# Kernel tuning notes

Hardware: AMD Instinct MI355X
Metric: run time of the kernel (lower is better)

The kernel has to match this reference:

```python
import jax, jax.numpy as jnp
import numpy as np

RADIUS = 0.4
K = 32
EPS = 1e-5


def ball_query(xyz, new_xyz, radius, k):
    """xyz: (B,N,3), new_xyz: (B,M,3) -> idx (B,M,k) int32.
    Replicates CUDA ball_query: first k points within radius (in index order),
    padded with the first found index."""
    N = xyz.shape[1]
    # squared distances (B,M,N)
    d2 = jnp.sum((new_xyz[:, :, None, :] - xyz[:, None, :, :]) ** 2, axis=-1)
    within = d2 < radius * radius
    order = jnp.arange(N, dtype=jnp.int32)
    key = jnp.where(within, order[None, None, :], N)
    idx_sorted = jnp.argsort(key, axis=-1)[..., :k].astype(jnp.int32)  # (B,M,k)
    cnt = within.sum(axis=-1)  # (B,M)
    first = idx_sorted[..., :1]
    slot = jnp.arange(k)[None, None, :]
    return jnp.where(slot < cnt[..., None], idx_sorted, first)


def gather_bmk(x_bnc, idx):
    """x_bnc: (B,N,C), idx: (B,M,K) -> (B,M,K,C)"""
    return jnp.take_along_axis(x_bnc[:, None, :, :], idx[..., None], axis=2)


def conv_bn_relu(x, w, b, gamma, beta):
    """x: (B,Cin,M,K); w: (Cout,Cin). 1x1 Conv2d + BatchNorm2d (train stats) + ReLU."""
    x = jnp.einsum('bcmk,oc->bomk', x, w) + b[None, :, None, None]
    mu = x.mean(axis=(0, 2, 3), keepdims=True)
    var = x.var(axis=(0, 2, 3), keepdims=True)
    x = gamma[None, :, None, None] * (x - mu) * jax.lax.rsqrt(var + EPS) + beta[None, :, None, None]
    return jax.nn.relu(x)


def setup_inputs() -> dict:
    key = jax.random.key(0)
    ks = jax.random.split(key, 16)
    B, N, C, M = 4, 16384, 128, 1024
    mlp = [131, 128, 128, 256]
    inp = {
        'points_xyz': jax.random.normal(ks[0], (B, N, 3), dtype=jnp.float32),
        'features': jax.random.normal(ks[1], (B, C, N), dtype=jnp.float32),
        'indices': jax.random.randint(ks[2], (B, M), 0, N, dtype=jnp.int32),
    }
    for i in range(3):
        cin, cout = mlp[i], mlp[i + 1]
        inp[f'w{i+1}'] = jax.random.normal(ks[3 + 4 * i], (cout, cin), dtype=jnp.float32) / np.sqrt(cin)
        inp[f'b{i+1}'] = jnp.zeros((cout,), dtype=jnp.float32)
        inp[f'g{i+1}'] = jnp.ones((cout,), dtype=jnp.float32)
        inp[f'beta{i+1}'] = jnp.zeros((cout,), dtype=jnp.float32)
    return inp


def reference(points_xyz, features, indices,
              w1, b1, g1, beta1, w2, b2, g2, beta2, w3, b3, g3, beta3):
    # sample centers: new_xyz (B,M,3)
    new_xyz = jnp.take_along_axis(points_xyz, indices[..., None], axis=1)
    # ball query + group
    idx = ball_query(points_xyz, new_xyz, RADIUS, K)            # (B,M,K)
    grouped_xyz = gather_bmk(points_xyz, idx) - new_xyz[:, :, None, :]  # (B,M,K,3)
    grouped_feat = gather_bmk(features.transpose(0, 2, 1), idx)         # (B,M,K,C)
    x = jnp.concatenate([grouped_xyz, grouped_feat], axis=-1)           # (B,M,K,3+C)
    x = x.transpose(0, 3, 1, 2)                                         # (B,3+C,M,K)
    # shared MLP (1x1 Conv2d + BN + ReLU)
    x = conv_bn_relu(x, w1, b1, g1, beta1)
    x = conv_bn_relu(x, w2, b2, g2, beta2)
    x = conv_bn_relu(x, w3, b3, g3, beta3)
    # max pool over K -> (B, Cout, M)
    new_features = x.max(axis=-1)
    return new_xyz, new_features
```

## Files before the change

### kernel.cpp

```cpp
#include <hip/hip_runtime.h>

#define B_ 4
#define N_ 16384
#define C_ 128
#define M_ 1024
#define K_ 32
#define NTOT (B_*M_*K_)
#define RAD2 0.16f
#define EPS_ 1e-5f

typedef unsigned short ushort_t;
typedef __bf16 bf16x8 __attribute__((ext_vector_type(8)));
typedef float f32x4 __attribute__((ext_vector_type(4)));

__device__ __forceinline__ float b2f(ushort_t u){
  unsigned int x = ((unsigned int)u) << 16;
  return __builtin_bit_cast(float, x);
}
__device__ __forceinline__ ushort_t f2b(float f){
  unsigned int u = __builtin_bit_cast(unsigned int, f);
  unsigned int r = (u + 0x7FFFu + ((u >> 16) & 1u)) >> 16;
  return (ushort_t)r;
}

__global__ __launch_bounds__(256) void ball_query_k(
    const float* __restrict__ xyz, const int* __restrict__ indices,
    float* __restrict__ new_xyz, int* __restrict__ idx)
{
  int t = threadIdx.x;
  int wv = t >> 6, lane = t & 63;
  int g = blockIdx.x*4 + wv;
  int b = g >> 10;
  const float* pb = xyz + (size_t)b*N_*3;
  const float4* pb4 = (const float4*)pb;
  int qi = indices[g];
  float qx = pb[qi*3+0], qy = pb[qi*3+1], qz = pb[qi*3+2];
  if (lane < 3) new_xyz[g*3 + lane] = pb[qi*3 + lane];

  int cnt = 0, firstIdx = 0;
  int* op = idx + g*K_;

  float4 buf0[6], buf1[6];
  #pragma unroll
  for (int i = 0; i < 6; i++) buf0[i] = pb4[lane*6 + i];

  auto process = [&](const float4* buf, int chunk){
    const float* f = (const float*)buf;
    unsigned int local_mask = 0;
    #pragma unroll
    for (int j = 0; j < 8; j++){
      float dx = f[j*3+0]-qx, dy = f[j*3+1]-qy, dz = f[j*3+2]-qz;
      if (dx*dx + dy*dy + dz*dz < RAD2) local_mask |= (1u << j);
    }
    if (__ballot(local_mask != 0) == 0ull) return;
    int base = chunk*512;
    int lcnt = __popc(local_mask);
    int incl = lcnt;
    #pragma unroll
    for (int d = 1; d < 64; d <<= 1){
      int tt = __shfl_up(incl, d);
      if (lane >= d) incl += tt;
    }
    int excl = incl - lcnt;
    int total = __shfl(incl, 63);
    if (cnt == 0){
      int lf = local_mask ? (lane*8 + __builtin_ctz(local_mask)) : 0x7fffffff;
      #pragma unroll
      for (int d = 1; d < 64; d <<= 1) lf = min(lf, __shfl_xor(lf, d));
      firstIdx = base + lf;
    }
    int sl = cnt + excl;
    unsigned int m = local_mask;
    while (m && sl < K_){
      int j = __builtin_ctz(m); m &= m - 1u;
      op[sl++] = base + lane*8 + j;
    }
    cnt += total;
  };

  for (int chunk = 0; chunk < 32; chunk += 2){
    if (chunk + 1 < 32){
      #pragma unroll
      for (int i = 0; i < 6; i++) buf1[i] = pb4[(chunk+1)*384 + lane*6 + i];
    }
    process(buf0, chunk);
    if (cnt >= K_) break;
    if (chunk + 2 < 32){
      #pragma unroll
      for (int i = 0; i < 6; i++) buf0[i] = pb4[(chunk+2)*384 + lane*6 + i];
    }
    process(buf1, chunk + 1);
    if (cnt >= K_) break;
  }
  if (cnt < K_){
    for (int s = cnt + lane; s < K_; s += 64) op[s] = firstIdx;
  }
}

__global__ __launch_bounds__(256) void transpose_feat_k(
    const float* __restrict__ feat, ushort_t* __restrict__ ftr_t)
{
  __shared__ float T[32][133];
  int bi = blockIdx.x;
  int b = bi >> 9, ntile = bi & 511;
  int n0 = ntile * 32;
  int t = threadIdx.x;
  int nl = t & 31;
  #pragma unroll
  for (int ci = 0; ci < 16; ci++){
    int c = ci*8 + (t >> 5);
    T[nl][c] = feat[((size_t)b*C_ + c)*N_ + n0 + nl];
  }
  __syncthreads();
  #pragma unroll
  for (int ii = 0; ii < 2; ii++){
    int v = ii*256 + t;
    int n2 = v >> 4, seg = v & 15;
    union { ushort_t u[8]; uint4 q; } pk;
    #pragma unroll
    for (int j = 0; j < 8; j++) pk.u[j] = f2b(T[n2][seg*8 + j]);
    *(uint4*)(ftr_t + ((size_t)b*N_ + n0 + n2)*C_ + seg*8) = pk.q;
  }
}

__global__ __launch_bounds__(256) void prep_w_k(
    const float* __restrict__ w1, const float* __restrict__ w2, const float* __restrict__ w3,
    ushort_t* __restrict__ W1b, ushort_t* __restrict__ W2b, ushort_t* __restrict__ W3b)
{
  const int T1 = 128*160, T2 = 128*128, T3 = 256*128;
  for (int e = blockIdx.x*256 + threadIdx.x; e < T1+T2+T3; e += gridDim.x*256){
    if (e < T1){
      int o = e / 160, c = e % 160;
      float v = 0.f;
      if (c < 128) v = w1[o*131 + 3 + c];
      else if (c < 131) v = w1[o*131 + (c - 128)];
      W1b[e] = f2b(v);
    } else if (e < T1+T2){
      int e2 = e - T1;
      W2b[e2] = f2b(w2[e2]);
    } else {
      int e3 = e - T1 - T2;
      W3b[e3] = f2b(w3[e3]);
    }
  }
}

__global__ __launch_bounds__(256, 2) void conv1_k(
    const float* __restrict__ xyz, const ushort_t* __restrict__ ftr_t,
    const int* __restrict__ idx, const float* __restrict__ new_xyz,
    const ushort_t* __restrict__ W1b, const float* __restrict__ b1,
    ushort_t* __restrict__ Y1, float* __restrict__ sumO, float* __restrict__ sqO)
{
  __shared__ alignas(16) ushort_t Xs[32*168];
  __shared__ alignas(16) float Ys[32*132];
  int t = threadIdx.x;
  int wv = t >> 6, lane = t & 63, quad = lane >> 4, l15 = lane & 15;
  int row = t >> 3, chunk = t & 7;

  if (t < 128){
    int rr = t >> 2, cc = t & 3;
    *(uint4*)(Xs + rr*168 + 128 + cc*8) = make_uint4(0,0,0,0);
  }
  bf16x8 wf[2][5];
  #pragma unroll
  for (int nt = 0; nt < 2; nt++)
    #pragma unroll
    for (int kt = 0; kt < 5; kt++)
      wf[nt][kt] = *(const bf16x8*)(W1b + (wv*32 + nt*16 + l15)*160 + kt*32 + quad*8);
  float bs_r[2] = { b1[wv*32 + l15], b1[wv*32 + 16 + l15] };
  float s[2] = {0.f,0.f}, s2[2] = {0.f,0.f};

  const int GPB = 8;
  int g0 = blockIdx.x * GPB;
  int b = g0 >> 10;
  int ia[GPB], ibv[GPB];
  #pragma unroll
  for (int i = 0; i < GPB; i++){
    ia[i]  = idx[(g0+i)*K_ + row];
    ibv[i] = idx[(g0+i)*K_ + (t & 31)];
  }
  for (int i = 0; i < GPB; i++){
    int g = g0 + i;
    const ushort_t* src = ftr_t + ((size_t)b*N_ + ia[i])*C_ + chunk*16;
    uint4 q0 = *(const uint4*)src;
    uint4 q1 = *(const uint4*)(src + 8);
    *(uint4*)(Xs + row*168 + chunk*16) = q0;
    *(uint4*)(Xs + row*168 + chunk*16 + 8) = q1;
    if (t < 32){
      const float* pp = xyz + ((size_t)b*N_ + ibv[i])*3;
      const float* qq = new_xyz + (size_t)g*3;
      unsigned int u0 = (unsigned int)f2b(pp[0]-qq[0]) | ((unsigned int)f2b(pp[1]-qq[1]) << 16);
      unsigned int u1 = (unsigned int)f2b(pp[2]-qq[2]);
      *(uint2*)(Xs + t*168 + 128) = make_uint2(u0, u1);
    }
    __syncthreads();
    bf16x8 af[2][5];
    #pragma unroll
    for (int mt = 0; mt < 2; mt++)
      #pragma unroll
      for (int kt = 0; kt < 5; kt++)
        af[mt][kt] = *(const bf16x8*)(Xs + (mt*16 + l15)*168 + kt*32 + quad*8);
    f32x4 acc[2][2];
    #pragma unroll
    for (int nt = 0; nt < 2; nt++){ acc[nt][0] = (f32x4){0,0,0,0}; acc[nt][1] = (f32x4){0,0,0,0}; }
    #pragma unroll
    for (int nt = 0; nt < 2; nt++)
      #pragma unroll
      for (int kt = 0; kt < 5; kt++){
        acc[nt][0] = __builtin_amdgcn_mfma_f32_16x16x32_bf16(af[0][kt], wf[nt][kt], acc[nt][0], 0,0,0);
        acc[nt][1] = __builtin_amdgcn_mfma_f32_16x16x32_bf16(af[1][kt], wf[nt][kt], acc[nt][1], 0,0,0);
      }
    #pragma unroll
    for (int nt = 0; nt < 2; nt++){
      int o = wv*32 + nt*16 + l15;
      #pragma unroll
      for (int mt = 0; mt < 2; mt++)
        #pragma unroll
        for (int r = 0; r < 4; r++){
          float v = acc[nt][mt][r] + bs_r[nt];
          s[nt] += v; s2[nt] += v*v;
          Ys[(mt*16 + quad*4 + r)*132 + o] = v;
        }
    }
    __syncthreads();
    {
      const float* yp = &Ys[row*132 + chunk*16];
      f32x4 y0 = *(const f32x4*)(yp);
      f32x4 y1 = *(const f32x4*)(yp + 4);
      f32x4 y2 = *(const f32x4*)(yp + 8);
      f32x4 y3 = *(const f32x4*)(yp + 12);
      union { ushort_t u[8]; uint4 q; } p0, p1;
      #pragma unroll
      for (int j = 0; j < 4; j++){
        p0.u[j] = f2b(y0[j]); p0.u[4+j] = f2b(y1[j]);
        p1.u[j] = f2b(y2[j]); p1.u[4+j] = f2b(y3[j]);
      }
      ushort_t* dst = Y1 + ((size_t)g*K_ + row)*128 + chunk*16;
      *(uint4*)dst = p0.q;
      *(uint4*)(dst + 8) = p1.q;
    }
  }
  #pragma unroll
  for (int nt = 0; nt < 2; nt++){
    s[nt]  += __shfl_xor(s[nt], 16);  s[nt]  += __shfl_xor(s[nt], 32);
    s2[nt] += __shfl_xor(s2[nt], 16); s2[nt] += __shfl_xor(s2[nt], 32);
    if (quad == 0){
      int o = wv*32 + nt*16 + l15;
      atomicAdd(&sumO[o], s[nt]);
      atomicAdd(&sqO[o], s2[nt]);
    }
  }
}

template<int COUT, bool MAXMIN>
__global__ __launch_bounds__(256, 2) void convB_k(
    const ushort_t* __restrict__ Yin, const ushort_t* __restrict__ Wb,
    const float* __restrict__ bias, const float* __restrict__ g_bn,
    const float* __restrict__ beta_bn, const float* __restrict__ sumI,
    const float* __restrict__ sqI, ushort_t* __restrict__ Yout,
    unsigned int* __restrict__ Ymm, float* __restrict__ sumO, float* __restrict__ sqO)
{
  constexpr int NT = COUT/64;
  constexpr int NXS = MAXMIN ? 2 : 1;
  __shared__ alignas(16) ushort_t Xs[NXS][32*136];
  __shared__ alignas(16) float Ys[MAXMIN ? 4 : 32*132];
  int t = threadIdx.x;
  int wv = t >> 6, lane = t & 63, quad = lane >> 4, l15 = lane & 15;
  int row = t >> 3, chunk = t & 7;

  float a_r[16], d_r[16];
  #pragma unroll
  for (int j = 0; j < 16; j++){
    int c = chunk*16 + j;
    float mu  = sumI[c] * (1.f/NTOT);
    float var = sqI[c]  * (1.f/NTOT) - mu*mu;
    float a = g_bn[c] * rsqrtf(var + EPS_);
    a_r[j] = a; d_r[j] = beta_bn[c] - a*mu;
  }
  bf16x8 wf[NT][4];
  #pragma unroll
  for (int nt = 0; nt < NT; nt++)
    #pragma unroll
    for (int kt = 0; kt < 4; kt++)
      wf[nt][kt] = *(const bf16x8*)(Wb + (wv*(NT*16) + nt*16 + l15)*128 + kt*32 + quad*8);
  float bs_r[NT];
  #pragma unroll
  for (int nt = 0; nt < NT; nt++) bs_r[nt] = bias[wv*(NT*16) + nt*16 + l15];
  float s[NT], s2[NT];
  #pragma unroll
  for (int nt = 0; nt < NT; nt++){ s[nt] = 0.f; s2[nt] = 0.f; }

  const int GPB = 8;
  int g0 = blockIdx.x * GPB;
  uint4 r0, r1;
  {
    const ushort_t* src = Yin + ((size_t)g0*K_ + row)*128 + chunk*16;
    r0 = *(const uint4*)src; r1 = *(const uint4*)(src + 8);
  }
  for (int i = 0; i < GPB; i++){
    int g = g0 + i;
    ushort_t* X = Xs[MAXMIN ? (i & (NXS-1)) : 0];
    union { ushort_t u[8]; uint4 q; } i0, i1, o0, o1;
    i0.q = r0; i1.q = r1;
    #pragma unroll
    for (int j = 0; j < 8; j++){
      o0.u[j] = f2b(fmaxf(a_r[j]  *b2f(i0.u[j]) + d_r[j],   0.f));
      o1.u[j] = f2b(fmaxf(a_r[8+j]*b2f(i1.u[j]) + d_r[8+j], 0.f));
    }
    *(uint4*)(X + row*136 + chunk*16) = o0.q;
    *(uint4*)(X + row*136 + chunk*16 + 8) = o1.q;
    if (i + 1 < GPB){
      const ushort_t* src = Yin + ((size_t)(g+1)*K_ + row)*128 + chunk*16;
      r0 = *(const uint4*)src; r1 = *(const uint4*)(src + 8);
    }
    __syncthreads();
    bf16x8 af[2][4];
    #pragma unroll
    for (int mt = 0; mt < 2; mt++)
      #pragma unroll
      for (int kt = 0; kt < 4; kt++)
        af[mt][kt] = *(const bf16x8*)(X + (mt*16 + l15)*136 + kt*32 + quad*8);
    f32x4 acc[NT][2];
    #pragma unroll
    for (int nt = 0; nt < NT; nt++){ acc[nt][0] = (f32x4){0,0,0,0}; acc[nt][1] = (f32x4){0,0,0,0}; }
    #pragma unroll
    for (int nt = 0; nt < NT; nt++)
      #pragma unroll
      for (int kt = 0; kt < 4; kt++){
        acc[nt][0] = __builtin_amdgcn_mfma_f32_16x16x32_bf16(af[0][kt], wf[nt][kt], acc[nt][0], 0,0,0);
        acc[nt][1] = __builtin_amdgcn_mfma_f32_16x16x32_bf16(af[1][kt], wf[nt][kt], acc[nt][1], 0,0,0);
      }
    if constexpr (!MAXMIN){
      #pragma unroll
      for (int nt = 0; nt < NT; nt++){
        int o = wv*(NT*16) + nt*16 + l15;
        #pragma unroll
        for (int mt = 0; mt < 2; mt++)
          #pragma unroll
          for (int r = 0; r < 4; r++){
            float v = acc[nt][mt][r] + bs_r[nt];
            s[nt] += v; s2[nt] += v*v;
            Ys[(mt*16 + quad*4 + r)*132 + o] = v;
          }
      }
      __syncthreads();
      const float* yp = &Ys[row*132 + chunk*16];
      f32x4 y0 = *(const f32x4*)(yp);
      f32x4 y1 = *(const f32x4*)(yp + 4);
      f32x4 y2 = *(const f32x4*)(yp + 8);
      f32x4 y3 = *(const f32x4*)(yp + 12);
      union { ushort_t u[8]; uint4 q; } p0, p1;
      #pragma unroll
      for (int j = 0; j < 4; j++){
        p0.u[j] = f2b(y0[j]); p0.u[4+j] = f2b(y1[j]);
        p1.u[j] = f2b(y2[j]); p1.u[4+j] = f2b(y3[j]);
      }
      ushort_t* dst = Yout + ((size_t)g*K_ + row)*128 + chunk*16;
      *(uint4*)dst = p0.q;
      *(uint4*)(dst + 8) = p1.q;
    } else {
      #pragma unroll
      for (int nt = 0; nt < NT; nt++){
        float v0 = acc[nt][0][0] + bs_r[nt];
        float mx = v0, mn = v0;
        s[nt] += v0; s2[nt] += v0*v0;
        #pragma unroll
        for (int mt = 0; mt < 2; mt++)
          #pragma unroll
          for (int r = 0; r < 4; r++){
            if (mt == 0 && r == 0) continue;
            float v = acc[nt][mt][r] + bs_r[nt];
            s[nt] += v; s2[nt] += v*v;
            mx = fmaxf(mx, v); mn = fminf(mn, v);
          }
        mx = fmaxf(mx, __shfl_xor(mx, 16)); mx = fmaxf(mx, __shfl_xor(mx, 32));
        mn = fminf(mn, __shfl_xor(mn, 16)); mn = fminf(mn, __shfl_xor(mn, 32));
        if (quad == 0){
          int o = wv*64 + nt*16 + l15;
          Ymm[(size_t)g*256 + o] = (unsigned int)f2b(mx) | ((unsigned int)f2b(mn) << 16);
        }
      }
    }
  }
  #pragma unroll
  for (int nt = 0; nt < NT; nt++){
    s[nt]  += __shfl_xor(s[nt], 16);  s[nt]  += __shfl_xor(s[nt], 32);
    s2[nt] += __shfl_xor(s2[nt], 16); s2[nt] += __shfl_xor(s2[nt], 32);
    if (quad == 0){
      int o = wv*(NT*16) + nt*16 + l15;
      atomicAdd(&sumO[o], s[nt]);
      atomicAdd(&sqO[o], s2[nt]);
    }
  }
}

__global__ __launch_bounds__(256) void finalize_k(
    const unsigned int* __restrict__ Ymm, const float* __restrict__ g3,
    const float* __restrict__ beta3, const float* __restrict__ sum3,
    const float* __restrict__ sq3, float* __restrict__ out)
{
  __shared__ float T[16][264];
  __shared__ float abn[256], dbn[256];
  int t = threadIdx.x;
  int b = blockIdx.x >> 6;
  int m0 = (blockIdx.x & 63) * 16;
  {
    float mu  = sum3[t] * (1.f/NTOT);
    float var = sq3[t]  * (1.f/NTOT) - mu*mu;
    float a = g3[t] * rsqrtf(var + EPS_);
    abn[t] = a; dbn[t] = beta3[t] - a*mu;
  }
  __syncthreads();
  #pragma unroll
  for (int i = 0; i < 4; i++){
    int v4 = i*256 + t;
    int m = v4 >> 6, oq = (v4 & 63) * 4;
    uint4 w = *(const uint4*)(Ymm + ((size_t)(b*M_ + m0 + m))*256 + oq);
    unsigned int wsv[4] = {w.x, w.y, w.z, w.w};
    float r[4];
    #pragma unroll
    for (int j = 0; j < 4; j++){
      int o = oq + j;
      float mx = b2f((ushort_t)(wsv[j] & 0xffffu));
      float mn = b2f((ushort_t)(wsv[j] >> 16));
      float a = abn[o];
      float val = (a >= 0.f) ? (a*mx + dbn[o]) : (a*mn + dbn[o]);
      r[j] = fmaxf(val, 0.f);
    }
    *(f32x4*)(&T[m][oq]) = *(f32x4*)r;
  }
  __syncthreads();
  #pragma unroll
  for (int p = 0; p < 4; p++){
    int o = p*64 + (t >> 2), c = t & 3;
    float4 v = make_float4(T[c*4+0][o], T[c*4+1][o], T[c*4+2][o], T[c*4+3][o]);
    *(float4*)(out + ((size_t)(b*256 + o))*M_ + m0 + c*4) = v;
  }
}

extern "C" void kernel_launch(void* const* d_in, const int* in_sizes, int n_in,
                              void* d_out, int out_size, void* d_ws, size_t ws_size,
                              hipStream_t stream)
{
  (void)in_sizes; (void)n_in; (void)out_size; (void)ws_size;
  const float* xyz  = (const float*)d_in[0];
  const float* feat = (const float*)d_in[1];
  const int*   inds = (const int*)d_in[2];
  const float* w1 = (const float*)d_in[3];
  const float* b1 = (const float*)d_in[4];
  const float* g1 = (const float*)d_in[5];
  const float* be1= (const float*)d_in[6];
  const float* w2 = (const float*)d_in[7];
  const float* b2 = (const float*)d_in[8];
  const float* g2 = (const float*)d_in[9];
  const float* be2= (const float*)d_in[10];
  const float* w3 = (const float*)d_in[11];
  const float* b3 = (const float*)d_in[12];
  const float* g3 = (const float*)d_in[13];
  const float* be3= (const float*)d_in[14];

  char* ws = (char*)d_ws;
  float* stats = (float*)ws;
  float* s1sum = stats + 0*256;  float* s1sq = stats + 1*256;
  float* s2sum = stats + 2*256;  float* s2sq = stats + 3*256;
  float* s3sum = stats + 4*256;  float* s3sq = stats + 5*256;
  size_t off = 6*256*sizeof(float);
  int* idx = (int*)(ws + off);                off += (size_t)B_*M_*K_*4;
  ushort_t* ftr_t = (ushort_t*)(ws + off);    off += (size_t)B_*N_*C_*2;
  ushort_t* W1b = (ushort_t*)(ws + off);      off += 128*160*2;
  ushort_t* W2b = (ushort_t*)(ws + off);      off += 128*128*2;
  ushort_t* W3b = (ushort_t*)(ws + off);      off += 256*128*2;
  ushort_t* Y1 = (ushort_t*)(ws + off);       off += (size_t)NTOT*128*2;
  ushort_t* Y2 = (ushort_t*)(ws + off);       off += (size_t)NTOT*128*2;
  unsigned int* Ymm = (unsigned int*)(ws + off); off += (size_t)B_*M_*256*4;

  float* new_xyz  = (float*)d_out;
  float* out_feat = (float*)d_out + (size_t)B_*M_*3;

  hipMemsetAsync(stats, 0, 6*256*sizeof(float), stream);
  prep_w_k<<<272, 256, 0, stream>>>(w1, w2, w3, W1b, W2b, W3b);
  transpose_feat_k<<<2048, 256, 0, stream>>>(feat, ftr_t);
  ball_query_k<<<1024, 256, 0, stream>>>(xyz, inds, new_xyz, idx);
  conv1_k<<<512, 256, 0, stream>>>(xyz, ftr_t, idx, new_xyz, W1b, b1, Y1, s1sum, s1sq);
  convB_k<128,false><<<512, 256, 0, stream>>>(Y1, W2b, b2, g1, be1, s1sum, s1sq, Y2, nullptr, s2sum, s2sq);
  convB_k<256,true ><<<512, 256, 0, stream>>>(Y2, W3b, b3, g2, be2, s2sum, s2sq, nullptr, Ymm, s3sum, s3sq);
  finalize_k<<<256, 256, 0, stream>>>(Ymm, g3, be3, s3sum, s3sq, out_feat);
}
```

Baseline: 225.0 us.

## Split conv output channels across two blocks to double grid size

Each conv kernel now covers half of the output channels per block, and the grid doubles from 512 to 1024 blocks. The goal is more parallelism and occupancy on a GPU with many CUs, plus less register and LDS pressure per block. The cost is that every block still gathers and normalizes the full 32x(128/160) input tile, so the gather and input-side work is done twice. Atomic stat updates per block also double.

```diff
diff --git a/kernel.cpp b/kernel.cpp
--- a/kernel.cpp
+++ b/kernel.cpp
@@ -152,26 +152,26 @@
     ushort_t* __restrict__ Y1, float* __restrict__ sumO, float* __restrict__ sqO)
 {
   __shared__ alignas(16) ushort_t Xs[32*168];
-  __shared__ alignas(16) float Ys[32*132];
+  __shared__ alignas(16) float Ys[32*68];
   int t = threadIdx.x;
   int wv = t >> 6, lane = t & 63, quad = lane >> 4, l15 = lane & 15;
   int row = t >> 3, chunk = t & 7;
+  int col0 = (blockIdx.x & 1) * 64;
+  int blk = blockIdx.x >> 1;
 
   if (t < 128){
     int rr = t >> 2, cc = t & 3;
     *(uint4*)(Xs + rr*168 + 128 + cc*8) = make_uint4(0,0,0,0);
   }
-  bf16x8 wf[2][5];
-  #pragma unroll
-  for (int nt = 0; nt < 2; nt++)
-    #pragma unroll
-    for (int kt = 0; kt < 5; kt++)
-      wf[nt][kt] = *(const bf16x8*)(W1b + (wv*32 + nt*16 + l15)*160 + kt*32 + quad*8);
-  float bs_r[2] = { b1[wv*32 + l15], b1[wv*32 + 16 + l15] };
-  float s[2] = {0.f,0.f}, s2[2] = {0.f,0.f};
+  bf16x8 wf[5];
+  #pragma unroll
+  for (int kt = 0; kt < 5; kt++)
+    wf[kt] = *(const bf16x8*)(W1b + (col0 + wv*16 + l15)*160 + kt*32 + quad*8);
+  float bs_r = b1[col0 + wv*16 + l15];
+  float s = 0.f, s2 = 0.f;
 
   const int GPB = 8;
-  int g0 = blockIdx.x * GPB;
+  int g0 = blk * GPB;
   int b = g0 >> 10;
   int ia[GPB], ibv[GPB];
   #pragma unroll
@@ -200,55 +200,42 @@
       #pragma unroll
       for (int kt = 0; kt < 5; kt++)
         af[mt][kt] = *(const bf16x8*)(Xs + (mt*16 + l15)*168 + kt*32 + quad*8);
-    f32x4 acc[2][2];
-    #pragma unroll
-    for (int nt = 0; nt < 2; nt++){ acc[nt][0] = (f32x4){0,0,0,0}; acc[nt][1] = (f32x4){0,0,0,0}; }
-    #pragma unroll
-    for (int nt = 0; nt < 2; nt++)
-      #pragma unroll
-      for (int kt = 0; kt < 5; kt++){
-        acc[nt][0] = __builtin_amdgcn_mfma_f32_16x16x32_bf16(af[0][kt], wf[nt][kt], acc[nt][0], 0,0,0);
-        acc[nt][1] = __builtin_amdgcn_mfma_f32_16x16x32_bf16(af[1][kt], wf[nt][kt], acc[nt][1], 0,0,0);
-      }
-    #pragma unroll
-    for (int nt = 0; nt < 2; nt++){
-      int o = wv*32 + nt*16 + l15;
+    f32x4 acc[2] = {(f32x4){0,0,0,0}, (f32x4){0,0,0,0}};
+    #pragma unroll
+    for (int kt = 0; kt < 5; kt++){
+      acc[0] = __builtin_amdgcn_mfma_f32_16x16x32_bf16(af[0][kt], wf[kt], acc[0], 0,0,0);
+      acc[1] = __builtin_amdgcn_mfma_f32_16x16x32_bf16(af[1][kt], wf[kt], acc[1], 0,0,0);
+    }
+    {
+      int o = wv*16 + l15;
       #pragma unroll
       for (int mt = 0; mt < 2; mt++)
         #pragma unroll
         for (int r = 0; r < 4; r++){
-          float v = acc[nt][mt][r] + bs_r[nt];
-          s[nt] += v; s2[nt] += v*v;
-          Ys[(mt*16 + quad*4 + r)*132 + o] = v;
+          float v = acc[mt][r] + bs_r;
+          s += v; s2 += v*v;
+          Ys[(mt*16 + quad*4 + r)*68 + o] = v;
         }
     }
     __syncthreads();
     {
-      const float* yp = &Ys[row*132 + chunk*16];
+      const float* yp = &Ys[row*68 + chunk*8];
       f32x4 y0 = *(const f32x4*)(yp);
       f32x4 y1 = *(const f32x4*)(yp + 4);
-      f32x4 y2 = *(const f32x4*)(yp + 8);
-      f32x4 y3 = *(const f32x4*)(yp + 12);
-      union { ushort_t u[8]; uint4 q; } p0, p1;
+      union { ushort_t u[8]; uint4 q; } p0;
       #pragma unroll
       for (int j = 0; j < 4; j++){
         p0.u[j] = f2b(y0[j]); p0.u[4+j] = f2b(y1[j]);
-        p1.u[j] = f2b(y2[j]); p1.u[4+j] = f2b(y3[j]);
       }
-      ushort_t* dst = Y1 + ((size_t)g*K_ + row)*128 + chunk*16;
-      *(uint4*)dst = p0.q;
-      *(uint4*)(dst + 8) = p1.q;
-    }
-  }
-  #pragma unroll
-  for (int nt = 0; nt < 2; nt++){
-    s[nt]  += __shfl_xor(s[nt], 16);  s[nt]  += __shfl_xor(s[nt], 32);
-    s2[nt] += __shfl_xor(s2[nt], 16); s2[nt] += __shfl_xor(s2[nt], 32);
-    if (quad == 0){
-      int o = wv*32 + nt*16 + l15;
-      atomicAdd(&sumO[o], s[nt]);
-      atomicAdd(&sqO[o], s2[nt]);
-    }
+      *(uint4*)(Y1 + ((size_t)g*K_ + row)*128 + col0 + chunk*8) = p0.q;
+    }
+  }
+  s  += __shfl_xor(s, 16);  s  += __shfl_xor(s, 32);
+  s2 += __shfl_xor(s2, 16); s2 += __shfl_xor(s2, 32);
+  if (quad == 0){
+    int o = col0 + wv*16 + l15;
+    atomicAdd(&sumO[o], s);
+    atomicAdd(&sqO[o], s2);
   }
 }
 
@@ -260,13 +247,16 @@
     const float* __restrict__ sqI, ushort_t* __restrict__ Yout,
     unsigned int* __restrict__ Ymm, float* __restrict__ sumO, float* __restrict__ sqO)
 {
-  constexpr int NT = COUT/64;
+  constexpr int HALF = COUT/2;
+  constexpr int NT = HALF/64;
   constexpr int NXS = MAXMIN ? 2 : 1;
   __shared__ alignas(16) ushort_t Xs[NXS][32*136];
-  __shared__ alignas(16) float Ys[MAXMIN ? 4 : 32*132];
+  __shared__ alignas(16) float Ys[MAXMIN ? 4 : 32*68];
   int t = threadIdx.x;
   int wv = t >> 6, lane = t & 63, quad = lane >> 4, l15 = lane & 15;
   int row = t >> 3, chunk = t & 7;
+  int col0 = (blockIdx.x & 1) * HALF;
+  int blk = blockIdx.x >> 1;
 
   float a_r[16], d_r[16];
   #pragma unroll
@@ -282,16 +272,16 @@
   for (int nt = 0; nt < NT; nt++)
     #pragma unroll
     for (int kt = 0; kt < 4; kt++)
-      wf[nt][kt] = *(const bf16x8*)(Wb + (wv*(NT*16) + nt*16 + l15)*128 + kt*32 + quad*8);
+      wf[nt][kt] = *(const bf16x8*)(Wb + (col0 + wv*(NT*16) + nt*16 + l15)*128 + kt*32 + quad*8);
   float bs_r[NT];
   #pragma unroll
-  for (int nt = 0; nt < NT; nt++) bs_r[nt] = bias[wv*(NT*16) + nt*16 + l15];
+  for (int nt = 0; nt < NT; nt++) bs_r[nt] = bias[col0 + wv*(NT*16) + nt*16 + l15];
   float s[NT], s2[NT];
   #pragma unroll
   for (int nt = 0; nt < NT; nt++){ s[nt] = 0.f; s2[nt] = 0.f; }
 
   const int GPB = 8;
-  int g0 = blockIdx.x * GPB;
+  int g0 = blk * GPB;
   uint4 r0, r1;
   {
     const ushort_t* src = Yin + ((size_t)g0*K_ + row)*128 + chunk*16;
@@ -331,33 +321,27 @@
         acc[nt][1] = __builtin_amdgcn_mfma_f32_16x16x32_bf16(af[1][kt], wf[nt][kt], acc[nt][1], 0,0,0);
       }
     if constexpr (!MAXMIN){
-      #pragma unroll
-      for (int nt = 0; nt < NT; nt++){
-        int o = wv*(NT*16) + nt*16 + l15;
+      {
+        int o = wv*16 + l15;
         #pragma unroll
         for (int mt = 0; mt < 2; mt++)
           #pragma unroll
           for (int r = 0; r < 4; r++){
-            float v = acc[nt][mt][r] + bs_r[nt];
-            s[nt] += v; s2[nt] += v*v;
-            Ys[(mt*16 + quad*4 + r)*132 + o] = v;
+            float v = acc[0][mt][r] + bs_r[0];
+            s[0] += v; s2[0] += v*v;
+            Ys[(mt*16 + quad*4 + r)*68 + o] = v;
           }
       }
       __syncthreads();
-      const float* yp = &Ys[row*132 + chunk*16];
+      const float* yp = &Ys[row*68 + chunk*8];
       f32x4 y0 = *(const f32x4*)(yp);
       f32x4 y1 = *(const f32x4*)(yp + 4);
-      f32x4 y2 = *(const f32x4*)(yp + 8);
-      f32x4 y3 = *(const f32x4*)(yp + 12);
-      union { ushort_t u[8]; uint4 q; } p0, p1;
+      union { ushort_t u[8]; uint4 q; } p0;
       #pragma unroll
       for (int j = 0; j < 4; j++){
         p0.u[j] = f2b(y0[j]); p0.u[4+j] = f2b(y1[j]);
-        p1.u[j] = f2b(y2[j]); p1.u[4+j] = f2b(y3[j]);
       }
-      ushort_t* dst = Yout + ((size_t)g*K_ + row)*128 + chunk*16;
-      *(uint4*)dst = p0.q;
-      *(uint4*)(dst + 8) = p1.q;
+      *(uint4*)(Yout + ((size_t)g*K_ + row)*128 + col0 + chunk*8) = p0.q;
     } else {
       #pragma unroll
       for (int nt = 0; nt < NT; nt++){
@@ -376,7 +360,7 @@
         mx = fmaxf(mx, __shfl_xor(mx, 16)); mx = fmaxf(mx, __shfl_xor(mx, 32));
         mn = fminf(mn, __shfl_xor(mn, 16)); mn = fminf(mn, __shfl_xor(mn, 32));
         if (quad == 0){
-          int o = wv*64 + nt*16 + l15;
+          int o = col0 + wv*(NT*16) + nt*16 + l15;
           Ymm[(size_t)g*256 + o] = (unsigned int)f2b(mx) | ((unsigned int)f2b(mn) << 16);
         }
       }
@@ -387,7 +371,7 @@
     s[nt]  += __shfl_xor(s[nt], 16);  s[nt]  += __shfl_xor(s[nt], 32);
     s2[nt] += __shfl_xor(s2[nt], 16); s2[nt] += __shfl_xor(s2[nt], 32);
     if (quad == 0){
-      int o = wv*(NT*16) + nt*16 + l15;
+      int o = col0 + wv*(NT*16) + nt*16 + l15;
       atomicAdd(&sumO[o], s[nt]);
       atomicAdd(&sqO[o], s2[nt]);
     }
@@ -481,8 +465,8 @@
   prep_w_k<<<272, 256, 0, stream>>>(w1, w2, w3, W1b, W2b, W3b);
   transpose_feat_k<<<2048, 256, 0, stream>>>(feat, ftr_t);
   ball_query_k<<<1024, 256, 0, stream>>>(xyz, inds, new_xyz, idx);
-  conv1_k<<<512, 256, 0, stream>>>(xyz, ftr_t, idx, new_xyz, W1b, b1, Y1, s1sum, s1sq);
-  convB_k<128,false><<<512, 256, 0, stream>>>(Y1, W2b, b2, g1, be1, s1sum, s1sq, Y2, nullptr, s2sum, s2sq);
-  convB_k<256,true ><<<512, 256, 0, stream>>>(Y2, W3b, b3, g2, be2, s2sum, s2sq, nullptr, Ymm, s3sum, s3sq);
+  conv1_k<<<1024, 256, 0, stream>>>(xyz, ftr_t, idx, new_xyz, W1b, b1, Y1, s1sum, s1sq);
+  convB_k<128,false><<<1024, 256, 0, stream>>>(Y1, W2b, b2, g1, be1, s1sum, s1sq, Y2, nullptr, s2sum, s2sq);
+  convB_k<256,true ><<<1024, 256, 0, stream>>>(Y2, W3b, b3, g2, be2, s2sum, s2sq, nullptr, Ymm, s3sum, s3sq);
   finalize_k<<<256, 256, 0, stream>>>(Ymm, g3, be3, s3sum, s3sq, out_feat);
 }
```

After: 221.4 us. About the same (-1.6%).
